# Kernel tuning notes

Measured on AMD Instinct MI355X. Metric: run time of the kernel, lower is better.

## Reference

```python
import jax, jax.numpy as jnp
from jax import lax
import numpy as np

ALIGN = 6                 # AlignW: pad width up to a multiple of align_width=6
W_BITS = 5
A_BITS = 5
A_MASK = (1 << A_BITS) - 1  # direct_conv2d bit-packs activations: keep low A_bits
DN = ('NCHW', 'OIHW', 'NCHW')


def _align_w(a):
    pad = (-a.shape[-1]) % ALIGN
    if pad:
        a = jnp.pad(a, ((0, 0), (0, 0), (0, 0), (0, pad)))
    return a


def _conv_relu(a, w, b):
    # nn.Conv2d(kernel_size=3, padding=2) + ReLU
    y = lax.conv_general_dilated(a, w, (1, 1), [(2, 2), (2, 2)], dimension_numbers=DN)
    return jax.nn.relu(y + b[None, :, None, None])


def _dc_conv(a, w):
    # DC_layer: integer direct conv2d, W_bits-quantized weights, A_bits activations,
    # stride 1, no padding (valid).
    aq = jnp.bitwise_and(a, A_MASK)
    return lax.conv_general_dilated(aq, w, (1, 1), [(0, 0), (0, 0)], dimension_numbers=DN,
                                    preferred_element_type=jnp.int32)


def _maxpool2(a):
    if jnp.issubdtype(a.dtype, jnp.floating):
        init = np.float32(-np.inf)
    else:
        init = np.int32(np.iinfo(np.int32).min)
    return lax.reduce_window(a, init, lax.max, (1, 1, 2, 2), (1, 1, 2, 2), 'VALID')


def _forward(x, ws, bs, qs, fc_w, fc_b):
    a = x
    k = 0
    for n in (2, 2, 3):          # float VGG blocks: [64,64,M, 128,128,M, 256,256,256,M]
        for _ in range(n):
            a = _conv_relu(_align_w(a), ws[k], bs[k])
            k += 1
        a = _maxpool2(a)
    # dequant stub is identity; x.int() truncates toward zero (a >= 0 after ReLU)
    xi = lax.stop_gradient(a).astype(jnp.int32)
    k = 0
    for n in (3, 3):             # DC blocks: [512,512,512,M, 512,512,512,M]
        for _ in range(n):
            xi = _dc_conv(_align_w(xi), qs[k])
            k += 1
        xi = _maxpool2(xi)
    # classifier: AdaptiveAvgPool2d((1,1)) + Flatten + Linear(512, 1000)
    pooled = jnp.mean(xi.astype(jnp.float32), axis=(2, 3))
    return pooled @ fc_w.T + fc_b


def setup_inputs() -> dict:
    key = jax.random.key(0)
    ks = jax.random.split(key, 24)
    d = {}
    d['x'] = jax.random.uniform(ks[0], (16, 3, 224, 224), jnp.float32) * 8.0
    conv_cfg = [(3, 64), (64, 64), (64, 128), (128, 128), (128, 256), (256, 256), (256, 256)]
    for i, (ci, co) in enumerate(conv_cfg):
        d[f'w{i + 1}'] = jax.random.normal(ks[1 + i], (co, ci, 3, 3), jnp.float32) * 0.1
        d[f'b{i + 1}'] = jax.random.normal(ks[8 + i], (co,), jnp.float32) * 0.1
    dc_cfg = [(256, 512)] + [(512, 512)] * 5
    for i, (ci, co) in enumerate(dc_cfg):
        # torch.randint(0, 2**W_bits - 1, ...) -> values in [0, 2**W_bits - 2]
        d[f'q{i + 1}'] = jax.random.randint(ks[15 + i], (co, ci, 3, 3), 0, 2 ** W_BITS - 1, jnp.int32)
    d['fc_w'] = jax.random.normal(ks[21], (1000, 512), jnp.float32) * 0.02
    d['fc_b'] = jnp.zeros((1000,), jnp.float32)
    return d


def reference(x, w1, w2, w3, w4, w5, w6, w7,
              b1, b2, b3, b4, b5, b6, b7,
              q1, q2, q3, q4, q5, q6, fc_w, fc_b):
    ws = (w1, w2, w3, w4, w5, w6, w7)
    bs = (b1, b2, b3, b4, b5, b6, b7)
    qs = (q1, q2, q3, q4, q5, q6)
    return _forward(x, ws, bs, qs, fc_w, fc_b)
```

## Files before the change

### kernel.cpp

```cpp
#include <hip/hip_runtime.h>
#include <cstddef>


typedef float v2f __attribute__((ext_vector_type(2)));

static __device__ __forceinline__ int dot4(int a, int b, int c) {
#if __has_builtin(__builtin_amdgcn_sdot4)
    return __builtin_amdgcn_sdot4(a, b, c, false);
#else
    return c + (a & 255) * (b & 255)
             + ((a >> 8) & 255) * ((b >> 8) & 255)
             + ((a >> 16) & 255) * ((b >> 16) & 255)
             + ((a >> 24) & 255) * ((b >> 24) & 255);
#endif
}

static __device__ __forceinline__ void ld6f(const float* __restrict__ p, float v[6]) {
    const float4 a = *reinterpret_cast<const float4*>(p);
    const float2 b = *reinterpret_cast<const float2*>(p + 4);
    v[0] = a.x; v[1] = a.y; v[2] = a.z; v[3] = a.w; v[4] = b.x; v[5] = b.y;
}
static __device__ __forceinline__ void ld6i(const int* __restrict__ p, int v[6]) {
    const int4 a = *reinterpret_cast<const int4*>(p);
    const int2 b = *reinterpret_cast<const int2*>(p + 4);
    v[0] = a.x; v[1] = a.y; v[2] = a.z; v[3] = a.w; v[4] = b.x; v[5] = b.y;
}

template<int CIN,int PH,int PW,int OH,int OW,int OPW,bool BORDER>
__global__ __launch_bounds__(256) void convf_k(
    const float* __restrict__ in, int instr,
    const float* __restrict__ wfp, const float* __restrict__ bias,
    float* __restrict__ out, int outstr, int total)
{
    constexpr int WB  = (OW + 3) / 4;
    constexpr int OPH = BORDER ? OH + 4 : OH;
    constexpr int OPL = OPH * OPW;
    const int s = blockIdx.x * 256 + threadIdx.x;
    if (s >= total) return;
    const int wb = s % WB;
    const int h  = (s / WB) % OH;
    const int n  = s / (WB * OH);
    const int w0 = wb * 4;
    const int cob = blockIdx.z;
    const int co0 = cob * 8;

    const float* ip = in + (size_t)n * instr + (size_t)h * PW + w0;
    const float* wl = wfp + (size_t)cob * CIN * 72;

    v2f acc[8][2];
#pragma unroll
    for (int c = 0; c < 8; ++c) { acc[c][0] = (v2f)0.f; acc[c][1] = (v2f)0.f; }

    float vb[3][6];
#pragma unroll
    for (int kh = 0; kh < 3; ++kh) ld6f(ip + kh * PW, vb[kh]);

#pragma unroll 2
    for (int ci = 0; ci < CIN; ++ci) {
        ip += PH * PW;
        float vn[3][6];
#pragma unroll
        for (int kh = 0; kh < 3; ++kh) ld6f(ip + kh * PW, vn[kh]);
        const float* wr = wl + ci * 72;
#pragma unroll
        for (int kh = 0; kh < 3; ++kh) {
            const v2f P0 = {vb[kh][0], vb[kh][1]};
            const v2f P1 = {vb[kh][1], vb[kh][2]};
            const v2f P2 = {vb[kh][2], vb[kh][3]};
            const v2f Q1 = {vb[kh][3], vb[kh][4]};
            const v2f Q2 = {vb[kh][4], vb[kh][5]};
#pragma unroll
            for (int c = 0; c < 8; ++c) {
                const float k0 = wr[c * 9 + kh * 3 + 0];
                const float k1 = wr[c * 9 + kh * 3 + 1];
                const float k2 = wr[c * 9 + kh * 3 + 2];
                const v2f k0p = {k0, k0}, k1p = {k1, k1}, k2p = {k2, k2};
                v2f a0 = acc[c][0];
                a0 = __builtin_elementwise_fma(P2, k2p, a0);
                a0 = __builtin_elementwise_fma(P1, k1p, a0);
                a0 = __builtin_elementwise_fma(P0, k0p, a0);
                acc[c][0] = a0;
                v2f a1 = acc[c][1];
                a1 = __builtin_elementwise_fma(Q2, k2p, a1);
                a1 = __builtin_elementwise_fma(Q1, k1p, a1);
                a1 = __builtin_elementwise_fma(P2, k0p, a1);
                acc[c][1] = a1;
            }
        }
#pragma unroll
        for (int kh = 0; kh < 3; ++kh)
#pragma unroll
            for (int j = 0; j < 6; ++j) vb[kh][j] = vn[kh][j];
    }

    float* ob = out + (size_t)n * outstr;
    const int ph  = BORDER ? h + 2 : h;
    const int pwo = BORDER ? 2 : 0;
#pragma unroll
    for (int c = 0; c < 8; ++c) {
        float* plane = ob + (size_t)(co0 + c) * OPL;
        float* row = plane + (size_t)ph * OPW;
        const float b = bias[co0 + c];
        float av[4] = {acc[c][0][0], acc[c][0][1], acc[c][1][0], acc[c][1][1]};
#pragma unroll
        for (int t = 0; t < 4; ++t)
            if (w0 + t < OW) { const float r = av[t] + b; row[pwo + w0 + t] = r > 0.f ? r : 0.f; }
        if (BORDER) {
            if (wb == 0) { row[0] = 0.f; row[1] = 0.f; }
            if (wb == WB - 1) { for (int pw = OW + 2; pw < OPW; ++pw) row[pw] = 0.f; }
            if (h == 0 || h == OH - 1) {
                float* r0 = plane + (h == 0 ? 0 : (size_t)(OH + 2) * OPW);
                for (int rr = 0; rr < 2; ++rr) {
                    float* br = r0 + (size_t)rr * OPW;
#pragma unroll
                    for (int t = 0; t < 4; ++t) if (w0 + t < OW) br[2 + w0 + t] = 0.f;
                    if (wb == 0) { br[0] = 0.f; br[1] = 0.f; }
                    if (wb == WB - 1) { for (int pw = OW + 2; pw < OPW; ++pw) br[pw] = 0.f; }
                }
            }
        }
    }
}

template<int CIN,int PH,int PW,int POH,int POW,int OPW,int OY,int OX,bool TOINT>
__global__ __launch_bounds__(256) void convfp_k(
    const float* __restrict__ in, int instr,
    const float* __restrict__ wfp, const float* __restrict__ bias,
    void* __restrict__ outv, int outstr, int total)
{
    constexpr int WBp = POW / 2;
    constexpr int OPH = POH + 2 * OY;
    constexpr int OPL = OPH * OPW;
    const int s = blockIdx.x * 256 + threadIdx.x;
    if (s >= total) return;
    const int pb = s % WBp;
    const int ph = (s / WBp) % POH;
    const int n  = s / (WBp * POH);
    const int cob = blockIdx.z;
    const int co0 = cob * 4;

    const float* ip = in + (size_t)n * instr + (size_t)(2 * ph) * PW + 4 * pb;
    const float* wl = wfp + (size_t)cob * CIN * 36;

    v2f acc[4][2][2];
#pragma unroll
    for (int c = 0; c < 4; ++c)
#pragma unroll
        for (int r = 0; r < 2; ++r) { acc[c][r][0] = (v2f)0.f; acc[c][r][1] = (v2f)0.f; }

    float vb[4][6];
#pragma unroll
    for (int r = 0; r < 4; ++r) ld6f(ip + r * PW, vb[r]);

    for (int ci = 0; ci < CIN; ++ci) {
        ip += PH * PW;
        float vn[4][6];
#pragma unroll
        for (int r = 0; r < 4; ++r) ld6f(ip + r * PW, vn[r]);
        const float* wr = wl + ci * 36;
#pragma unroll
        for (int r = 0; r < 2; ++r) {
#pragma unroll
            for (int kh = 0; kh < 3; ++kh) {
                const float* vv = vb[r + kh];
                const v2f P0 = {vv[0], vv[1]};
                const v2f P1 = {vv[1], vv[2]};
                const v2f P2 = {vv[2], vv[3]};
                const v2f Q1 = {vv[3], vv[4]};
                const v2f Q2 = {vv[4], vv[5]};
#pragma unroll
                for (int c = 0; c < 4; ++c) {
                    const float k0 = wr[c * 9 + kh * 3 + 0];
                    const float k1 = wr[c * 9 + kh * 3 + 1];
                    const float k2 = wr[c * 9 + kh * 3 + 2];
                    const v2f k0p = {k0, k0}, k1p = {k1, k1}, k2p = {k2, k2};
                    v2f a0 = acc[c][r][0];
                    a0 = __builtin_elementwise_fma(P2, k2p, a0);
                    a0 = __builtin_elementwise_fma(P1, k1p, a0);
                    a0 = __builtin_elementwise_fma(P0, k0p, a0);
                    acc[c][r][0] = a0;
                    v2f a1 = acc[c][r][1];
                    a1 = __builtin_elementwise_fma(Q2, k2p, a1);
                    a1 = __builtin_elementwise_fma(Q1, k1p, a1);
                    a1 = __builtin_elementwise_fma(P2, k0p, a1);
                    acc[c][r][1] = a1;
                }
            }
        }
#pragma unroll
        for (int r = 0; r < 4; ++r)
#pragma unroll
            for (int j = 0; j < 6; ++j) vb[r][j] = vn[r][j];
    }

#pragma unroll
    for (int c = 0; c < 4; ++c) {
        const float b = bias[co0 + c];
        float r00 = acc[c][0][0][0] + b; r00 = r00 > 0.f ? r00 : 0.f;
        float r01 = acc[c][0][0][1] + b; r01 = r01 > 0.f ? r01 : 0.f;
        float r02 = acc[c][0][1][0] + b; r02 = r02 > 0.f ? r02 : 0.f;
        float r03 = acc[c][0][1][1] + b; r03 = r03 > 0.f ? r03 : 0.f;
        float r10 = acc[c][1][0][0] + b; r10 = r10 > 0.f ? r10 : 0.f;
        float r11 = acc[c][1][0][1] + b; r11 = r11 > 0.f ? r11 : 0.f;
        float r12 = acc[c][1][1][0] + b; r12 = r12 > 0.f ? r12 : 0.f;
        float r13 = acc[c][1][1][1] + b; r13 = r13 > 0.f ? r13 : 0.f;
        float p0 = r00; p0 = p0 > r01 ? p0 : r01; p0 = p0 > r10 ? p0 : r10; p0 = p0 > r11 ? p0 : r11;
        float p1 = r02; p1 = p1 > r03 ? p1 : r03; p1 = p1 > r12 ? p1 : r12; p1 = p1 > r13 ? p1 : r13;

        if constexpr (TOINT) {
            int* plane = (int*)outv + (size_t)n * outstr + (size_t)(co0 + c) * OPL;
            int* row = plane + (size_t)(OY + ph) * OPW;
            row[OX + 2 * pb]     = (int)p0;
            row[OX + 2 * pb + 1] = (int)p1;
            if (pb == WBp - 1) { for (int pw = OX + POW; pw < OPW; ++pw) row[pw] = 0; }
        } else {
            float* plane = (float*)outv + (size_t)n * outstr + (size_t)(co0 + c) * OPL;
            float* row = plane + (size_t)(OY + ph) * OPW;
            row[OX + 2 * pb]     = p0;
            row[OX + 2 * pb + 1] = p1;
            if (OX > 0 && pb == 0) { row[0] = 0.f; row[1] = 0.f; }
            if (pb == WBp - 1) { for (int pw = OX + POW; pw < OPW; ++pw) row[pw] = 0.f; }
            if (OY > 0 && (ph == 0 || ph == POH - 1)) {
                float* r0 = plane + (ph == 0 ? 0 : (size_t)(OY + POH) * OPW);
                for (int rr = 0; rr < OY; ++rr) {
                    float* br = r0 + (size_t)rr * OPW;
                    br[OX + 2 * pb] = 0.f; br[OX + 2 * pb + 1] = 0.f;
                    if (pb == 0) { br[0] = 0.f; br[1] = 0.f; }
                    if (pb == WBp - 1) { for (int pw = OX + POW; pw < OPW; ++pw) br[pw] = 0.f; }
                }
            }
        }
    }
}

template<int CIN4,int PH,int PW,int OH,int OW,int OPW,bool PACKOUT>
__global__ __launch_bounds__(256) void convq_k(
    const int* __restrict__ in, int instr, const int* __restrict__ wqp,
    int* __restrict__ out, int outstr, int total)
{
    constexpr int WB  = (OW + 3) / 4;
    constexpr int OPL = OH * OPW;
    const int s = blockIdx.x * 256 + threadIdx.x;
    if (s >= total) return;
    const int wb = s % WB;
    const int h  = (s / WB) % OH;
    const int n  = s / (WB * OH);
    const int w0 = wb * 4;
    const int cob = blockIdx.z;
    const int co0 = cob * 8;

    const int* ip = in + (size_t)n * instr + (size_t)h * PW + w0;
    const int* wl = wqp + (size_t)cob * CIN4 * 72;

    int acc[8][4];
#pragma unroll
    for (int c = 0; c < 8; ++c)
#pragma unroll
        for (int t = 0; t < 4; ++t) acc[c][t] = 0;

    int vb[3][6];
#pragma unroll
    for (int kh = 0; kh < 3; ++kh) ld6i(ip + kh * PW, vb[kh]);

#pragma unroll 2
    for (int ci = 0; ci < CIN4; ++ci) {
        ip += PH * PW;
        int vn[3][6];
#pragma unroll
        for (int kh = 0; kh < 3; ++kh) ld6i(ip + kh * PW, vn[kh]);
        const int* wr = wl + ci * 72;
#pragma unroll
        for (int kh = 0; kh < 3; ++kh) {
#pragma unroll
            for (int c = 0; c < 8; ++c) {
                const int k0 = wr[c * 9 + kh * 3 + 0];
                const int k1 = wr[c * 9 + kh * 3 + 1];
                const int k2 = wr[c * 9 + kh * 3 + 2];
#pragma unroll
                for (int t = 0; t < 4; ++t)
                    acc[c][t] = dot4(vb[kh][t], k0,
                                dot4(vb[kh][t + 1], k1,
                                dot4(vb[kh][t + 2], k2, acc[c][t])));
            }
        }
#pragma unroll
        for (int kh = 0; kh < 3; ++kh)
#pragma unroll
            for (int j = 0; j < 6; ++j) vb[kh][j] = vn[kh][j];
    }

    if (PACKOUT) {
        int* base = out + (size_t)n * outstr + (size_t)(cob * 2) * OPL + (size_t)h * OPW + w0;
#pragma unroll
        for (int t = 0; t < 4; ++t) {
            if (w0 + t < OW) {
                const int lo = (acc[0][t] & 31) | ((acc[1][t] & 31) << 8)
                             | ((acc[2][t] & 31) << 16) | ((acc[3][t] & 31) << 24);
                const int hi = (acc[4][t] & 31) | ((acc[5][t] & 31) << 8)
                             | ((acc[6][t] & 31) << 16) | ((acc[7][t] & 31) << 24);
                base[t] = lo;
                base[OPL + t] = hi;
            }
        }
        if (wb == WB - 1) {
            for (int pw = OW; pw < OPW; ++pw) { base[pw - w0] = 0; base[OPL + pw - w0] = 0; }
        }
    } else {
        int* ob = out + (size_t)n * outstr;
#pragma unroll
        for (int c = 0; c < 8; ++c) {
            int* row = ob + (size_t)(co0 + c) * OPL + (size_t)h * OPW;
#pragma unroll
            for (int t = 0; t < 4; ++t)
                if (w0 + t < OW) row[w0 + t] = acc[c][t];
            if (wb == WB - 1) { for (int pw = OW; pw < OPW; ++pw) row[pw] = 0; }
        }
    }
}

__global__ void pack_wf_k(const float* __restrict__ w, float* __restrict__ out,
                          int CIN, int TC, int total)
{
    const int i = blockIdx.x * 256 + threadIdx.x;
    if (i >= total) return;
    const int r = i % 9;
    const int c = (i / 9) % TC;
    const int t = i / (9 * TC);
    const int ci = t % CIN;
    const int cob = t / CIN;
    out[i] = w[(((size_t)cob * TC + c) * CIN + ci) * 9 + r];
}

__global__ void pack_wq_k(const int* __restrict__ q, int* __restrict__ out,
                          int CIN4, int total)
{
    const int i = blockIdx.x * 256 + threadIdx.x;
    if (i >= total) return;
    const int r = i % 9;
    const int c = (i / 9) % 8;
    const int t = i / 72;
    const int ci4 = t % CIN4;
    const int cob = t / CIN4;
    const int co = cob * 8 + c;
    const int* p = q + ((size_t)co * CIN4 * 4 + ci4 * 4) * 9 + r;
    out[i] = (p[0] & 255) | ((p[9] & 255) << 8) | ((p[18] & 255) << 16) | ((p[27] & 255) << 24);
}

template<int CIN,int PH,int PW>
__global__ void pack_a_k(const int* __restrict__ in, int instr,
                         int* __restrict__ out, int outstr, int total)
{
    const int i = blockIdx.x * 256 + threadIdx.x;
    if (i >= total) return;
    constexpr int CIN4 = CIN / 4;
    constexpr int PL = PH * PW;
    int t = i;
    const int pw = t % PW; t /= PW;
    const int ph = t % PH; t /= PH;
    const int c4 = t % CIN4; const int n = t / CIN4;
    const int* p = in + (size_t)n * instr + ((size_t)(c4 * 4) * PH + ph) * PW + pw;
    out[(size_t)n * outstr + ((size_t)c4 * PH + ph) * PW + pw] =
        (p[0] & 31) | ((p[PL] & 31) << 8) | ((p[2 * PL] & 31) << 16) | ((p[3 * PL] & 31) << 24);
}

template<int C,int HI,int WI,int HO,int WO,int OPH,int OPW>
__global__ void pool_i_k(const int* __restrict__ in, int instr,
                         int* __restrict__ out, int outstr, int total)
{
    const int i = blockIdx.x * 256 + threadIdx.x;
    if (i >= total) return;
    constexpr int OPL = OPH * OPW;
    int t = i;
    const int px = t % OPW; t /= OPW;
    const int py = t % OPH; t /= OPH;
    const int c  = t % C;   const int n = t / C;
    int v = 0;
    if (py < HO && px < WO) {
        const int* p = in + (size_t)n * instr + ((size_t)c * HI + 2 * py) * WI + 2 * px;
        int m = p[0];
        m = m > p[1] ? m : p[1];
        m = m > p[WI] ? m : p[WI];
        m = m > p[WI + 1] ? m : p[WI + 1];
        v = m;
    }
    out[(size_t)n * outstr + (size_t)c * OPL + (size_t)py * OPW + px] = v;
}

__global__ void copyin_k(const float* __restrict__ x, float* __restrict__ dst,
                         int outstr, int total)
{
    const int i = blockIdx.x * 256 + threadIdx.x;
    if (i >= total) return;
    int t = i;
    const int pw = t % 232; t /= 232;
    const int ph = t % 228; t /= 228;
    const int c  = t % 3;   const int n = t / 3;
    float v = 0.f;
    const int y = ph - 2, xx = pw - 2;
    if ((unsigned)y < 224u && (unsigned)xx < 224u)
        v = x[(size_t)n * 150528 + ((size_t)c * 224 + y) * 224 + xx];
    dst[(size_t)n * outstr + ((size_t)c * 228 + ph) * 232 + pw] = v;
}

__global__ void pool_mean_k(const int* __restrict__ in, int instr,
                            float* __restrict__ out, int outstr, int total)
{
    const int i = blockIdx.x * 256 + threadIdx.x;
    if (i >= total) return;
    const int n = i / 512, c = i % 512;
    const int* p = in + (size_t)n * instr + (size_t)c * 33;
    int s = 0;
#pragma unroll
    for (int j = 0; j < 33; ++j) s += p[j];
    out[(size_t)n * outstr + c] = (float)s / 33.0f;
}

__global__ void fc_k(const float* __restrict__ pooled, const float* __restrict__ w,
                     const float* __restrict__ b, float* __restrict__ out,
                     int nb, int n0)
{
    const int i = blockIdx.x * 256 + threadIdx.x;
    if (i >= nb * 1000) return;
    const int co = i % 1000;
    const int n  = i / 1000;
    const float* pv = pooled + (size_t)n * 512;
    const float* wr = w + (size_t)co * 512;
    float s = b[co];
    for (int c = 0; c < 512; ++c) s = fmaf(pv[c], wr[c], s);
    out[(size_t)(n0 + n) * 1000 + co] = s;
}

extern "C" void kernel_launch(void* const* d_in, const int* in_sizes, int n_in,
                              void* d_out, int out_size, void* d_ws, size_t ws_size,
                              hipStream_t stream)
{
    (void)n_in; (void)out_size;
    const float* x = (const float*)d_in[0];
    const float* W[7]; const float* Bv[7]; const int* Q[6];
    const bool inter = (in_sizes[2] == 64);
    for (int i = 0; i < 7; ++i) {
        if (inter) { W[i] = (const float*)d_in[1 + 2 * i]; Bv[i] = (const float*)d_in[2 + 2 * i]; }
        else       { W[i] = (const float*)d_in[1 + i];     Bv[i] = (const float*)d_in[8 + i];     }
    }
    for (int i = 0; i < 6; ++i) Q[i] = (const int*)d_in[15 + i];
    const float* fcw = (const float*)d_in[21];
    const float* fcb = (const float*)d_in[22];
    float* outp = (float*)d_out;

    static const int FCO[7]  = {64, 64, 128, 128, 256, 256, 256};
    static const int FCIN[7] = {3, 64, 64, 128, 128, 256, 256};
    static const int FTC[7]  = {8, 4, 8, 4, 8, 8, 4};
    static const int QCIN4[6] = {64, 128, 128, 128, 128, 128};
    size_t wfoff[7], wft = 0;
    for (int i = 0; i < 7; ++i) { wfoff[i] = wft; wft += (size_t)FCO[i] * FCIN[i] * 9; }
    size_t wqoff[6], wqt = 0;
    for (int i = 0; i < 6; ++i) { wqoff[i] = wqt; wqt += (size_t)512 * QCIN4[i] * 9 * 4; }
    const size_t WTOT = wft + wqt;

    float* wfb = (float*)d_ws;
    int*   wqb = (int*)((float*)d_ws + wft);
    for (int i = 0; i < 7; ++i) {
        const int total = FCO[i] * FCIN[i] * 9;
        pack_wf_k<<<(total + 255) / 256, 256, 0, stream>>>(W[i], wfb + wfoff[i], FCIN[i], FTC[i], total);
    }
    for (int i = 0; i < 6; ++i) {
        const int total = 512 * QCIN4[i] * 9;
        pack_wq_k<<<(total + 255) / 256, 256, 0, stream>>>(Q[i], wqb + wqoff[i], QCIN4[i], total);
    }

    const long long SZ_X0 = 158688,  SZ_F1 = 3532800, SZ_P1 = 936448;
    const long long SZ_F4 = 2027520, SZ_P2 = 580608,  SZ_F7 = 1264640;
    const long long SZ_F8 = 1440768, SZ_I0 = 360448,  SZ_PK1 = 90112;
    const long long SZ_D1 = 168960,  SZ_D2 = 157696,  SZ_D3 = 532480;
    const long long SZ_P4 = 159744,  SZ_PK4 = 39936,  SZ_D4 = 33792;
    const long long SZ_D5 = 27648,   SZ_D6 = 86016,   SZ_P5 = 16896;

    float* AR = (float*)d_ws + WTOT;
    long long AE2 = ((long long)(ws_size / 4) - (long long)WTOT - 20480) & ~3LL;

    int nbB = 16;
    for (;; nbB >>= 1) {
        if (nbB == 1) break;
        const long long f = nbB;
        const long long low = (nbB == 16) ? 0 : SZ_P1 * 16;
        const bool ok = (SZ_P1 * 16 + SZ_F4 * f <= AE2)
                     && (low + SZ_P2 * f <= AE2 - SZ_F4 * f)
                     && (low + SZ_F8 * f <= AE2 - SZ_F7 * f)
                     && (low + (SZ_PK1 + SZ_D1 + SZ_D2 + SZ_D3) * f <= AE2);
        if (ok) break;
    }
    int cA = 16;
    while (cA > 1 && SZ_P1 * 16 + (SZ_X0 + SZ_F1) * cA > AE2) cA >>= 1;

    const long long lowb = (nbB == 16) ? 0 : SZ_P1 * 16;
    float* tP1 = AR;
    float* tX0 = AR + SZ_P1 * 16;
    float* tF1 = tX0 + SZ_X0 * cA;
    float* tF4 = AR + (AE2 - SZ_F4 * nbB);
    float* tP2 = AR + lowb;
    float* tF7 = AR + (AE2 - SZ_F7 * nbB);
    float* tF8 = AR + lowb;
    int*   tI0 = (int*)(AR + (AE2 - SZ_I0 * nbB));
    int*   tPK1 = (int*)(AR + lowb);
    int*   tD1 = tPK1 + SZ_PK1 * nbB;
    int*   tD2 = tD1 + SZ_D1 * nbB;
    int*   tD3 = tD2 + SZ_D2 * nbB;
    int*   tP4 = (int*)(AR + lowb);
    int*   tPK4 = tP4 + SZ_P4 * nbB;
    int*   tD4 = tPK4 + SZ_PK4 * nbB;
    int*   tD5 = tD4 + SZ_D4 * nbB;
    int*   tD6 = tD5 + SZ_D5 * nbB;
    int*   tP5 = (int*)(AR + lowb);
    float* tPP = (float*)(tP5 + SZ_P5 * nbB);

    for (int a0 = 0; a0 < 16; a0 += cA) {
        const int nb = cA;
        {
            const int total = nb * 3 * 228 * 232;
            copyin_k<<<(total + 255) / 256, 256, 0, stream>>>(
                x + (size_t)a0 * 150528, tX0, (int)SZ_X0, total);
        }
        {
            const int total = nb * 226 * 58;
            dim3 g((total + 255) / 256, 1, 8);
            convf_k<3, 228, 232, 226, 230, 240, true><<<g, 256, 0, stream>>>(
                tX0, (int)SZ_X0, wfb + wfoff[0], Bv[0], tF1, (int)SZ_F1, total);
        }
        {
            const int total = nb * 114 * 59;
            dim3 g((total + 255) / 256, 1, 16);
            convfp_k<64, 230, 240, 114, 118, 124, 2, 2, false><<<g, 256, 0, stream>>>(
                tF1, (int)SZ_F1, wfb + wfoff[1], Bv[1],
                tP1 + (size_t)a0 * SZ_P1, (int)SZ_P1, total);
        }
    }

    for (int b0 = 0; b0 < 16; b0 += nbB) {
        const int nb = nbB;
        {
            const int total = nb * 116 * 31;
            dim3 g((total + 255) / 256, 1, 16);
            convf_k<64, 118, 124, 116, 122, 132, true><<<g, 256, 0, stream>>>(
                tP1 + (size_t)b0 * SZ_P1, (int)SZ_P1, wfb + wfoff[2], Bv[2],
                tF4, (int)SZ_F4, total);
        }
        {
            const int total = nb * 59 * 32;
            dim3 g((total + 255) / 256, 1, 32);
            convfp_k<128, 120, 132, 59, 64, 72, 2, 2, false><<<g, 256, 0, stream>>>(
                tF4, (int)SZ_F4, wfb + wfoff[3], Bv[3], tP2, (int)SZ_P2, total);
        }
        {
            const int total = nb * 61 * 17;
            dim3 g((total + 255) / 256, 1, 32);
            convf_k<128, 63, 72, 61, 68, 76, true><<<g, 256, 0, stream>>>(
                tP2, (int)SZ_P2, wfb + wfoff[4], Bv[4], tF7, (int)SZ_F7, total);
        }
        {
            const int total = nb * 63 * 19;
            dim3 g((total + 255) / 256, 1, 32);
            convf_k<256, 65, 76, 63, 74, 84, true><<<g, 256, 0, stream>>>(
                tF7, (int)SZ_F7, wfb + wfoff[5], Bv[5], tF8, (int)SZ_F8, total);
        }
        {
            const int total = nb * 32 * 20;
            dim3 g((total + 255) / 256, 1, 64);
            convfp_k<256, 67, 84, 32, 40, 44, 0, 0, true><<<g, 256, 0, stream>>>(
                tF8, (int)SZ_F8, wfb + wfoff[6], Bv[6], (void*)tI0, (int)SZ_I0, total);
        }
        {
            const int total = nb * 64 * 32 * 44;
            pack_a_k<256, 32, 44><<<(total + 255) / 256, 256, 0, stream>>>(
                tI0, (int)SZ_I0, tPK1, (int)SZ_PK1, total);
        }
        {
            const int total = nb * 30 * 10;
            dim3 g((total + 255) / 256, 1, 64);
            convq_k<64, 32, 44, 30, 40, 44, true><<<g, 256, 0, stream>>>(
                tPK1, (int)SZ_PK1, wqb + wqoff[0], tD1, (int)SZ_D1, total);
        }
        {
            const int total = nb * 28 * 10;
            dim3 g((total + 255) / 256, 1, 64);
            convq_k<128, 30, 44, 28, 40, 44, true><<<g, 256, 0, stream>>>(
                tD1, (int)SZ_D1, wqb + wqoff[1], tD2, (int)SZ_D2, total);
        }
        {
            const int total = nb * 26 * 10;
            dim3 g((total + 255) / 256, 1, 64);
            convq_k<128, 28, 44, 26, 40, 40, false><<<g, 256, 0, stream>>>(
                tD2, (int)SZ_D2, wqb + wqoff[2], tD3, (int)SZ_D3, total);
        }
        {
            const int total = nb * 512 * 13 * 24;
            pool_i_k<512, 26, 40, 13, 20, 13, 24><<<(total + 255) / 256, 256, 0, stream>>>(
                tD3, (int)SZ_D3, tP4, (int)SZ_P4, total);
        }
        {
            const int total = nb * 128 * 13 * 24;
            pack_a_k<512, 13, 24><<<(total + 255) / 256, 256, 0, stream>>>(
                tP4, (int)SZ_P4, tPK4, (int)SZ_PK4, total);
        }
        {
            const int total = nb * 11 * 6;
            dim3 g((total + 255) / 256, 1, 64);
            convq_k<128, 13, 24, 11, 22, 24, true><<<g, 256, 0, stream>>>(
                tPK4, (int)SZ_PK4, wqb + wqoff[3], tD4, (int)SZ_D4, total);
        }
        {
            const int total = nb * 9 * 6;
            dim3 g((total + 255) / 256, 1, 64);
            convq_k<128, 11, 24, 9, 22, 24, true><<<g, 256, 0, stream>>>(
                tD4, (int)SZ_D4, wqb + wqoff[4], tD5, (int)SZ_D5, total);
        }
        {
            const int total = nb * 7 * 6;
            dim3 g((total + 255) / 256, 1, 64);
            convq_k<128, 9, 24, 7, 22, 24, false><<<g, 256, 0, stream>>>(
                tD5, (int)SZ_D5, wqb + wqoff[5], tD6, (int)SZ_D6, total);
        }
        {
            const int total = nb * 512 * 33;
            pool_i_k<512, 7, 24, 3, 11, 3, 11><<<(total + 255) / 256, 256, 0, stream>>>(
                tD6, (int)SZ_D6, tP5, (int)SZ_P5, total);
        }
        {
            const int total = nb * 512;
            pool_mean_k<<<(total + 255) / 256, 256, 0, stream>>>(
                tP5, (int)SZ_P5, tPP, 512, total);
        }
        {
            const int total = nb * 1000;
            fc_k<<<(total + 255) / 256, 256, 0, stream>>>(tPP, fcw, fcb, outp, nb, b0);
        }
    }
}
```

Before: 6.185 ms.

## Swap grid axes so channel blocks vary fastest; manually double-buffer channel loops

Moves the output-channel-block index to blockIdx.x and the spatial index to blockIdx.z, so consecutively scheduled workgroups share the same input tile across channel blocks, which should improve L2 reuse of activations. It also replaces the copy-based register rotation in the conv inner loops with explicit ping-pong buffers across two input channels, removing the register moves and letting loads overlap compute. The cost is a somewhat larger register footprint, and the loops now assume an even channel count in the convfp and convq kernels.

```diff
diff --git a/kernel.cpp b/kernel.cpp
--- a/kernel.cpp
+++ b/kernel.cpp
@@ -26,6 +26,92 @@
     v[0] = a.x; v[1] = a.y; v[2] = a.z; v[3] = a.w; v[4] = b.x; v[5] = b.y;
 }
 
+static __device__ __forceinline__ void fmac8(const float v[3][6],
+                                             const float* __restrict__ wr,
+                                             v2f acc[8][2])
+{
+#pragma unroll
+    for (int kh = 0; kh < 3; ++kh) {
+        const v2f P0 = {v[kh][0], v[kh][1]};
+        const v2f P1 = {v[kh][1], v[kh][2]};
+        const v2f P2 = {v[kh][2], v[kh][3]};
+        const v2f Q1 = {v[kh][3], v[kh][4]};
+        const v2f Q2 = {v[kh][4], v[kh][5]};
+#pragma unroll
+        for (int c = 0; c < 8; ++c) {
+            const float k0 = wr[c * 9 + kh * 3 + 0];
+            const float k1 = wr[c * 9 + kh * 3 + 1];
+            const float k2 = wr[c * 9 + kh * 3 + 2];
+            const v2f k0p = {k0, k0}, k1p = {k1, k1}, k2p = {k2, k2};
+            v2f a0 = acc[c][0];
+            a0 = __builtin_elementwise_fma(P2, k2p, a0);
+            a0 = __builtin_elementwise_fma(P1, k1p, a0);
+            a0 = __builtin_elementwise_fma(P0, k0p, a0);
+            acc[c][0] = a0;
+            v2f a1 = acc[c][1];
+            a1 = __builtin_elementwise_fma(Q2, k2p, a1);
+            a1 = __builtin_elementwise_fma(Q1, k1p, a1);
+            a1 = __builtin_elementwise_fma(P2, k0p, a1);
+            acc[c][1] = a1;
+        }
+    }
+}
+
+static __device__ __forceinline__ void fmac4p(const float v[4][6],
+                                              const float* __restrict__ wr,
+                                              v2f acc[4][2][2])
+{
+#pragma unroll
+    for (int r = 0; r < 2; ++r) {
+#pragma unroll
+        for (int kh = 0; kh < 3; ++kh) {
+            const float* vv = v[r + kh];
+            const v2f P0 = {vv[0], vv[1]};
+            const v2f P1 = {vv[1], vv[2]};
+            const v2f P2 = {vv[2], vv[3]};
+            const v2f Q1 = {vv[3], vv[4]};
+            const v2f Q2 = {vv[4], vv[5]};
+#pragma unroll
+            for (int c = 0; c < 4; ++c) {
+                const float k0 = wr[c * 9 + kh * 3 + 0];
+                const float k1 = wr[c * 9 + kh * 3 + 1];
+                const float k2 = wr[c * 9 + kh * 3 + 2];
+                const v2f k0p = {k0, k0}, k1p = {k1, k1}, k2p = {k2, k2};
+                v2f a0 = acc[c][r][0];
+                a0 = __builtin_elementwise_fma(P2, k2p, a0);
+                a0 = __builtin_elementwise_fma(P1, k1p, a0);
+                a0 = __builtin_elementwise_fma(P0, k0p, a0);
+                acc[c][r][0] = a0;
+                v2f a1 = acc[c][r][1];
+                a1 = __builtin_elementwise_fma(Q2, k2p, a1);
+                a1 = __builtin_elementwise_fma(Q1, k1p, a1);
+                a1 = __builtin_elementwise_fma(P2, k0p, a1);
+                acc[c][r][1] = a1;
+            }
+        }
+    }
+}
+
+static __device__ __forceinline__ void dotc8(const int v[3][6],
+                                             const int* __restrict__ wr,
+                                             int acc[8][4])
+{
+#pragma unroll
+    for (int kh = 0; kh < 3; ++kh) {
+#pragma unroll
+        for (int c = 0; c < 8; ++c) {
+            const int k0 = wr[c * 9 + kh * 3 + 0];
+            const int k1 = wr[c * 9 + kh * 3 + 1];
+            const int k2 = wr[c * 9 + kh * 3 + 2];
+#pragma unroll
+            for (int t = 0; t < 4; ++t)
+                acc[c][t] = dot4(v[kh][t], k0,
+                            dot4(v[kh][t + 1], k1,
+                            dot4(v[kh][t + 2], k2, acc[c][t])));
+        }
+    }
+}
+
 template<int CIN,int PH,int PW,int OH,int OW,int OPW,bool BORDER>
 __global__ __launch_bounds__(256) void convf_k(
     const float* __restrict__ in, int instr,
@@ -35,13 +121,13 @@
     constexpr int WB  = (OW + 3) / 4;
     constexpr int OPH = BORDER ? OH + 4 : OH;
     constexpr int OPL = OPH * OPW;
-    const int s = blockIdx.x * 256 + threadIdx.x;
+    const int s = blockIdx.z * 256 + threadIdx.x;
     if (s >= total) return;
     const int wb = s % WB;
     const int h  = (s / WB) % OH;
     const int n  = s / (WB * OH);
     const int w0 = wb * 4;
-    const int cob = blockIdx.z;
+    const int cob = blockIdx.x;
     const int co0 = cob * 8;
 
     const float* ip = in + (size_t)n * instr + (size_t)h * PW + w0;
@@ -51,46 +137,32 @@
 #pragma unroll
     for (int c = 0; c < 8; ++c) { acc[c][0] = (v2f)0.f; acc[c][1] = (v2f)0.f; }
 
-    float vb[3][6];
+    float vb[3][6], vn[3][6];
 #pragma unroll
     for (int kh = 0; kh < 3; ++kh) ld6f(ip + kh * PW, vb[kh]);
 
-#pragma unroll 2
-    for (int ci = 0; ci < CIN; ++ci) {
-        ip += PH * PW;
-        float vn[3][6];
-#pragma unroll
-        for (int kh = 0; kh < 3; ++kh) ld6f(ip + kh * PW, vn[kh]);
-        const float* wr = wl + ci * 72;
-#pragma unroll
-        for (int kh = 0; kh < 3; ++kh) {
-            const v2f P0 = {vb[kh][0], vb[kh][1]};
-            const v2f P1 = {vb[kh][1], vb[kh][2]};
-            const v2f P2 = {vb[kh][2], vb[kh][3]};
-            const v2f Q1 = {vb[kh][3], vb[kh][4]};
-            const v2f Q2 = {vb[kh][4], vb[kh][5]};
-#pragma unroll
-            for (int c = 0; c < 8; ++c) {
-                const float k0 = wr[c * 9 + kh * 3 + 0];
-                const float k1 = wr[c * 9 + kh * 3 + 1];
-                const float k2 = wr[c * 9 + kh * 3 + 2];
-                const v2f k0p = {k0, k0}, k1p = {k1, k1}, k2p = {k2, k2};
-                v2f a0 = acc[c][0];
-                a0 = __builtin_elementwise_fma(P2, k2p, a0);
-                a0 = __builtin_elementwise_fma(P1, k1p, a0);
-                a0 = __builtin_elementwise_fma(P0, k0p, a0);
-                acc[c][0] = a0;
-                v2f a1 = acc[c][1];
-                a1 = __builtin_elementwise_fma(Q2, k2p, a1);
-                a1 = __builtin_elementwise_fma(Q1, k1p, a1);
-                a1 = __builtin_elementwise_fma(P2, k0p, a1);
-                acc[c][1] = a1;
-            }
-        }
-#pragma unroll
-        for (int kh = 0; kh < 3; ++kh)
-#pragma unroll
-            for (int j = 0; j < 6; ++j) vb[kh][j] = vn[kh][j];
+    if constexpr ((CIN & 1) == 0) {
+        for (int ci = 0; ci < CIN; ci += 2) {
+            ip += PH * PW;
+#pragma unroll
+            for (int kh = 0; kh < 3; ++kh) ld6f(ip + kh * PW, vn[kh]);
+            fmac8(vb, wl + (size_t)ci * 72, acc);
+            ip += PH * PW;
+#pragma unroll
+            for (int kh = 0; kh < 3; ++kh) ld6f(ip + kh * PW, vb[kh]);
+            fmac8(vn, wl + (size_t)(ci + 1) * 72, acc);
+        }
+    } else {
+        for (int ci = 0; ci < CIN; ++ci) {
+            ip += PH * PW;
+#pragma unroll
+            for (int kh = 0; kh < 3; ++kh) ld6f(ip + kh * PW, vn[kh]);
+            fmac8(vb, wl + (size_t)ci * 72, acc);
+#pragma unroll
+            for (int kh = 0; kh < 3; ++kh)
+#pragma unroll
+                for (int j = 0; j < 6; ++j) vb[kh][j] = vn[kh][j];
+        }
     }
 
     float* ob = out + (size_t)n * outstr;
@@ -131,12 +203,12 @@
     constexpr int WBp = POW / 2;
     constexpr int OPH = POH + 2 * OY;
     constexpr int OPL = OPH * OPW;
-    const int s = blockIdx.x * 256 + threadIdx.x;
+    const int s = blockIdx.z * 256 + threadIdx.x;
     if (s >= total) return;
     const int pb = s % WBp;
     const int ph = (s / WBp) % POH;
     const int n  = s / (WBp * POH);
-    const int cob = blockIdx.z;
+    const int cob = blockIdx.x;
     const int co0 = cob * 4;
 
     const float* ip = in + (size_t)n * instr + (size_t)(2 * ph) * PW + 4 * pb;
@@ -148,49 +220,19 @@
 #pragma unroll
         for (int r = 0; r < 2; ++r) { acc[c][r][0] = (v2f)0.f; acc[c][r][1] = (v2f)0.f; }
 
-    float vb[4][6];
+    float vb[4][6], vn[4][6];
 #pragma unroll
     for (int r = 0; r < 4; ++r) ld6f(ip + r * PW, vb[r]);
 
-    for (int ci = 0; ci < CIN; ++ci) {
+    for (int ci = 0; ci < CIN; ci += 2) {
         ip += PH * PW;
-        float vn[4][6];
 #pragma unroll
         for (int r = 0; r < 4; ++r) ld6f(ip + r * PW, vn[r]);
-        const float* wr = wl + ci * 36;
-#pragma unroll
-        for (int r = 0; r < 2; ++r) {
-#pragma unroll
-            for (int kh = 0; kh < 3; ++kh) {
-                const float* vv = vb[r + kh];
-                const v2f P0 = {vv[0], vv[1]};
-                const v2f P1 = {vv[1], vv[2]};
-                const v2f P2 = {vv[2], vv[3]};
-                const v2f Q1 = {vv[3], vv[4]};
-                const v2f Q2 = {vv[4], vv[5]};
-#pragma unroll
-                for (int c = 0; c < 4; ++c) {
-                    const float k0 = wr[c * 9 + kh * 3 + 0];
-                    const float k1 = wr[c * 9 + kh * 3 + 1];
-                    const float k2 = wr[c * 9 + kh * 3 + 2];
-                    const v2f k0p = {k0, k0}, k1p = {k1, k1}, k2p = {k2, k2};
-                    v2f a0 = acc[c][r][0];
-                    a0 = __builtin_elementwise_fma(P2, k2p, a0);
-                    a0 = __builtin_elementwise_fma(P1, k1p, a0);
-                    a0 = __builtin_elementwise_fma(P0, k0p, a0);
-                    acc[c][r][0] = a0;
-                    v2f a1 = acc[c][r][1];
-                    a1 = __builtin_elementwise_fma(Q2, k2p, a1);
-                    a1 = __builtin_elementwise_fma(Q1, k1p, a1);
-                    a1 = __builtin_elementwise_fma(P2, k0p, a1);
-                    acc[c][r][1] = a1;
-                }
-            }
-        }
-#pragma unroll
-        for (int r = 0; r < 4; ++r)
-#pragma unroll
-            for (int j = 0; j < 6; ++j) vb[r][j] = vn[r][j];
+        fmac4p(vb, wl + (size_t)ci * 36, acc);
+        ip += PH * PW;
+#pragma unroll
+        for (int r = 0; r < 4; ++r) ld6f(ip + r * PW, vb[r]);
+        fmac4p(vn, wl + (size_t)(ci + 1) * 36, acc);
     }
 
 #pragma unroll
@@ -240,13 +282,13 @@
 {
     constexpr int WB  = (OW + 3) / 4;
     constexpr int OPL = OH * OPW;
-    const int s = blockIdx.x * 256 + threadIdx.x;
+    const int s = blockIdx.z * 256 + threadIdx.x;
     if (s >= total) return;
     const int wb = s % WB;
     const int h  = (s / WB) % OH;
     const int n  = s / (WB * OH);
     const int w0 = wb * 4;
-    const int cob = blockIdx.z;
+    const int cob = blockIdx.x;
     const int co0 = cob * 8;
 
     const int* ip = in + (size_t)n * instr + (size_t)h * PW + w0;
@@ -258,35 +300,19 @@
 #pragma unroll
         for (int t = 0; t < 4; ++t) acc[c][t] = 0;
 
-    int vb[3][6];
+    int vb[3][6], vn[3][6];
 #pragma unroll
     for (int kh = 0; kh < 3; ++kh) ld6i(ip + kh * PW, vb[kh]);
 
-#pragma unroll 2
-    for (int ci = 0; ci < CIN4; ++ci) {
+    for (int ci = 0; ci < CIN4; ci += 2) {
         ip += PH * PW;
-        int vn[3][6];
 #pragma unroll
         for (int kh = 0; kh < 3; ++kh) ld6i(ip + kh * PW, vn[kh]);
-        const int* wr = wl + ci * 72;
-#pragma unroll
-        for (int kh = 0; kh < 3; ++kh) {
-#pragma unroll
-            for (int c = 0; c < 8; ++c) {
-                const int k0 = wr[c * 9 + kh * 3 + 0];
-                const int k1 = wr[c * 9 + kh * 3 + 1];
-                const int k2 = wr[c * 9 + kh * 3 + 2];
-#pragma unroll
-                for (int t = 0; t < 4; ++t)
-                    acc[c][t] = dot4(vb[kh][t], k0,
-                                dot4(vb[kh][t + 1], k1,
-                                dot4(vb[kh][t + 2], k2, acc[c][t])));
-            }
-        }
-#pragma unroll
-        for (int kh = 0; kh < 3; ++kh)
-#pragma unroll
-            for (int j = 0; j < 6; ++j) vb[kh][j] = vn[kh][j];
+        dotc8(vb, wl + (size_t)ci * 72, acc);
+        ip += PH * PW;
+#pragma unroll
+        for (int kh = 0; kh < 3; ++kh) ld6i(ip + kh * PW, vb[kh]);
+        dotc8(vn, wl + (size_t)(ci + 1) * 72, acc);
     }
 
     if (PACKOUT) {
@@ -522,13 +548,13 @@
         }
         {
             const int total = nb * 226 * 58;
-            dim3 g((total + 255) / 256, 1, 8);
+            dim3 g(8, 1, (total + 255) / 256);
             convf_k<3, 228, 232, 226, 230, 240, true><<<g, 256, 0, stream>>>(
                 tX0, (int)SZ_X0, wfb + wfoff[0], Bv[0], tF1, (int)SZ_F1, total);
         }
         {
             const int total = nb * 114 * 59;
-            dim3 g((total + 255) / 256, 1, 16);
+            dim3 g(16, 1, (total + 255) / 256);
             convfp_k<64, 230, 240, 114, 118, 124, 2, 2, false><<<g, 256, 0, stream>>>(
                 tF1, (int)SZ_F1, wfb + wfoff[1], Bv[1],
                 tP1 + (size_t)a0 * SZ_P1, (int)SZ_P1, total);
@@ -539,32 +565,32 @@
         const int nb = nbB;
         {
             const int total = nb * 116 * 31;
-            dim3 g((total + 255) / 256, 1, 16);
+            dim3 g(16, 1, (total + 255) / 256);
             convf_k<64, 118, 124, 116, 122, 132, true><<<g, 256, 0, stream>>>(
                 tP1 + (size_t)b0 * SZ_P1, (int)SZ_P1, wfb + wfoff[2], Bv[2],
                 tF4, (int)SZ_F4, total);
         }
         {
             const int total = nb * 59 * 32;
-            dim3 g((total + 255) / 256, 1, 32);
+            dim3 g(32, 1, (total + 255) / 256);
             convfp_k<128, 120, 132, 59, 64, 72, 2, 2, false><<<g, 256, 0, stream>>>(
                 tF4, (int)SZ_F4, wfb + wfoff[3], Bv[3], tP2, (int)SZ_P2, total);
         }
         {
             const int total = nb * 61 * 17;
-            dim3 g((total + 255) / 256, 1, 32);
+            dim3 g(32, 1, (total + 255) / 256);
             convf_k<128, 63, 72, 61, 68, 76, true><<<g, 256, 0, stream>>>(
                 tP2, (int)SZ_P2, wfb + wfoff[4], Bv[4], tF7, (int)SZ_F7, total);
         }
         {
             const int total = nb * 63 * 19;
-            dim3 g((total + 255) / 256, 1, 32);
+            dim3 g(32, 1, (total + 255) / 256);
             convf_k<256, 65, 76, 63, 74, 84, true><<<g, 256, 0, stream>>>(
                 tF7, (int)SZ_F7, wfb + wfoff[5], Bv[5], tF8, (int)SZ_F8, total);
         }
         {
             const int total = nb * 32 * 20;
-            dim3 g((total + 255) / 256, 1, 64);
+            dim3 g(64, 1, (total + 255) / 256);
             convfp_k<256, 67, 84, 32, 40, 44, 0, 0, true><<<g, 256, 0, stream>>>(
                 tF8, (int)SZ_F8, wfb + wfoff[6], Bv[6], (void*)tI0, (int)SZ_I0, total);
         }
@@ -575,19 +601,19 @@
         }
         {
             const int total = nb * 30 * 10;
-            dim3 g((total + 255) / 256, 1, 64);
+            dim3 g(64, 1, (total + 255) / 256);
             convq_k<64, 32, 44, 30, 40, 44, true><<<g, 256, 0, stream>>>(
                 tPK1, (int)SZ_PK1, wqb + wqoff[0], tD1, (int)SZ_D1, total);
         }
         {
             const int total = nb * 28 * 10;
-            dim3 g((total + 255) / 256, 1, 64);
+            dim3 g(64, 1, (total + 255) / 256);
             convq_k<128, 30, 44, 28, 40, 44, true><<<g, 256, 0, stream>>>(
                 tD1, (int)SZ_D1, wqb + wqoff[1], tD2, (int)SZ_D2, total);
         }
         {
             const int total = nb * 26 * 10;
-            dim3 g((total + 255) / 256, 1, 64);
+            dim3 g(64, 1, (total + 255) / 256);
             convq_k<128, 28, 44, 26, 40, 40, false><<<g, 256, 0, stream>>>(
                 tD2, (int)SZ_D2, wqb + wqoff[2], tD3, (int)SZ_D3, total);
         }
@@ -603,19 +629,19 @@
         }
         {
             const int total = nb * 11 * 6;
-            dim3 g((total + 255) / 256, 1, 64);
+            dim3 g(64, 1, (total + 255) / 256);
             convq_k<128, 13, 24, 11, 22, 24, true><<<g, 256, 0, stream>>>(
                 tPK4, (int)SZ_PK4, wqb + wqoff[3], tD4, (int)SZ_D4, total);
         }
         {
             const int total = nb * 9 * 6;
-            dim3 g((total + 255) / 256, 1, 64);
+            dim3 g(64, 1, (total + 255) / 256);
             convq_k<128, 11, 24, 9, 22, 24, true><<<g, 256, 0, stream>>>(
                 tD4, (int)SZ_D4, wqb + wqoff[4], tD5, (int)SZ_D5, total);
         }
         {
             const int total = nb * 7 * 6;
-            dim3 g((total + 255) / 256, 1, 64);
+            dim3 g(64, 1, (total + 255) / 256);
             convq_k<128, 9, 24, 7, 22, 24, false><<<g, 256, 0, stream>>>(
                 tD5, (int)SZ_D5, wqb + wqoff[5], tD6, (int)SZ_D6, total);
         }
```

Measured after the change: 5.998 ms. 1.03x faster.
